# Optimization experiments

Measured on AMD Instinct MI355X. Metric: run time of the kernel, lower is better.

## Reference

```python
import jax, jax.numpy as jnp
from jax import lax
import numpy as np

B = 2048
NUM_COMPO = 650
NUM_CHARS = 27533
COMPO_SCORE_THRESH = 0.7
SCORE_ADJ_SCALE = 0.1
K = 10  # top-k chars and max padded hit indices


def setup_inputs() -> dict:
    key = jax.random.key(0)
    k1, k2, k3, k4, k5 = jax.random.split(key, 5)
    return {
        "pred_class_logits": jax.random.normal(k1, (B, NUM_CHARS), dtype=jnp.float32),
        "pred_compo_logits": jax.random.normal(k2, (B, NUM_COMPO), dtype=jnp.float32),
        "chinese_char_ids": jax.random.randint(k3, (B,), 0, NUM_CHARS, dtype=jnp.int32),
        "compo_co_occurrence_prob": jax.random.uniform(k4, (NUM_COMPO, NUM_COMPO), dtype=jnp.float32),
        "compo_chinese_matrix": jax.random.randint(k5, (NUM_COMPO, NUM_CHARS), 0, 2, dtype=jnp.int32),
    }


def _components_to_char(compo_scores, co_occ, matrix):
    """Per-sample: compo_scores [C], co_occ [C,C], matrix [C,V] (0/1 int)."""
    # score adjustment: sum over compos with score>0.88 of co_occ row * score * scale
    hi = compo_scores > 0.88
    w = jnp.where(hi, compo_scores, 0.0)                       # [C]
    adjusted = compo_scores + SCORE_ADJ_SCALE * (w @ co_occ)   # [C]
    max_idx = jnp.argmax(adjusted)
    max_score = compo_scores[max_idx]

    # select compos above threshold, sorted descending by score
    sel = compo_scores > COMPO_SCORE_THRESH
    num_sel = jnp.sum(sel.astype(jnp.int32))
    masked = jnp.where(sel, compo_scores, -jnp.inf)
    order = jnp.argsort(-masked)                                # selected first, desc
    sorted_scores = jnp.take(compo_scores, order)               # [C]

    hit0 = matrix[max_idx]                                      # [V] int

    def cond(st):
        i, hit, _prev = st
        return (i < num_sel) & (jnp.sum(hit) > 1)

    def body(st):
        i, hit, _prev = st
        comp = matrix[order[i]]
        new_hit = ((hit + comp) == 2).astype(hit.dtype)         # intersection
        return (i + 1, new_hit, hit)

    i, hit, prev = lax.while_loop(cond, body, (jnp.int32(1), hit0, hit0))
    num_hit = jnp.sum(hit)
    empty = num_hit == 0
    i = jnp.where(empty, i - 1, i)
    hit = jnp.where(empty, prev, hit)
    hit_score = jnp.where(i == 1, max_score, sorted_scores[i - 1])

    # first K indices where hit == 1, padded with -1 (fixed shape)
    ar = jnp.arange(NUM_CHARS, dtype=jnp.int32)
    vals = jnp.where(hit == 1, NUM_CHARS - ar, 0)
    topv, topi = lax.top_k(vals, K)
    hit_indices = jnp.where(topv > 0, topi.astype(jnp.int32), -1)
    return adjusted, hit_indices, hit_score


def reference(pred_class_logits, pred_compo_logits, chinese_char_ids,
              compo_co_occurrence_prob, compo_chinese_matrix):
    class_probs = jax.nn.softmax(pred_class_logits, axis=1)     # [B, V]
    compo_scores = jax.nn.sigmoid(pred_compo_logits)            # [B, C]
    class_scores, class_indices = lax.top_k(class_probs, K)     # [B, K]

    adjusted, hit_idx, hit_scores = jax.vmap(
        _components_to_char, in_axes=(0, None, None)
    )(compo_scores, compo_co_occurrence_prob, compo_chinese_matrix)

    num_hit = jnp.sum((hit_idx != -1).astype(jnp.int32), axis=1)  # [B]
    pred1 = jnp.where(num_hit == 1, hit_idx[:, 0], class_indices[:, 0])
    pred2 = jnp.where((class_scores[:, 0] < 0.85) & (num_hit == 1),
                      hit_idx[:, 0], class_indices[:, 0])

    hit_compare = jnp.any(class_indices[:, :, None] == hit_idx[:, None, :], axis=2)  # [B,K]
    j = jnp.argmax(hit_compare, axis=1)  # first True (all-False -> 0), matches stable desc argsort[0]
    pred3 = class_indices[jnp.arange(class_indices.shape[0]), j]

    return (class_indices, class_scores, compo_scores, adjusted,
            hit_idx, hit_scores, pred1, pred2, pred3)
```

## Files before the change

### kernel.cpp

```cpp
#include <hip/hip_runtime.h>
#include <math.h>

#define NB 2048
#define NC 650
#define NV 27533
#define NK 10
#define NWRD 861
#define NT 256
#define NCHUNK 11
#define CHPR 431
#define SVCAP 768

__global__ __launch_bounds__(NT) void pack_kernel(const int* __restrict__ mat,
                                                  unsigned* __restrict__ packed) {
  const int c = blockIdx.x >> 1;
  const int half = blockIdx.x & 1;
  const int lane = threadIdx.x & 63;
  const int w4 = threadIdx.x >> 6;
  const int ch0 = half ? 216 : 0;
  const int ch1 = half ? CHPR : 216;
  const int* row = mat + (size_t)c * NV;
  const size_t obase = (size_t)c * NWRD;

  int ch = ch0 + w4;
  int val = 0;
  if (ch < ch1) {
    int e = (ch << 6) + lane;
    val = (e < NV) ? row[e] : 0;
  }
  while (ch < ch1) {
    int chn = ch + 4;
    int valn = 0;
    if (chn < ch1) {
      int en = (chn << 6) + lane;
      valn = (en < NV) ? row[en] : 0;
    }
    unsigned long long m = __ballot(val != 0);
    if (lane < 2) {
      int wi = (ch << 1) + lane;
      if (wi < NWRD) packed[obase + wi] = (unsigned)(m >> (lane * 32));
    }
    val = valn;
    ch = chn;
  }
}

__device__ __forceinline__ int block_sum(int v, volatile int* red4, int tid) {
#pragma unroll
  for (int off = 32; off > 0; off >>= 1) v += __shfl_down(v, off);
  if ((tid & 63) == 0) red4[tid >> 6] = v;
  __syncthreads();
  int tot = red4[0] + red4[1] + red4[2] + red4[3];
  __syncthreads();
  return tot;
}

__global__ __launch_bounds__(NT, 8) void gen_pred_kernel(
    const float* __restrict__ class_logits,
    const float* __restrict__ compo_logits,
    const float* __restrict__ co_occ,
    const unsigned* __restrict__ packed,
    float* __restrict__ out) {
  const int b = blockIdx.x;
  const int tid = threadIdx.x;
  const int lane = tid & 63;
  const int wid = tid >> 6;

  __shared__ __align__(16) char arena[10464];
  float* s_sv_v = (float*)arena;
  int* s_sv_i = (int*)(arena + 3072);
  float* s_score = (float*)arena;
  int* s_selidx = (int*)(arena + 2608);
  int* s_hi = (int*)(arena + 5216);
  int* s_order = (int*)(arena + 7824);

  __shared__ float red_f[4];
  __shared__ float red_s[4];
  __shared__ int red_i[4];
  __shared__ int s_svcnt;
  __shared__ int s_cls_idx[NK];
  __shared__ float s_cls_sc[NK];
  __shared__ int s_hit[NK];
  __shared__ int s_hicnt[NCHUNK];
  __shared__ int s_selcnt[NCHUNK];

  const size_t o_cidx = 0;
  const size_t o_csc = (size_t)NB * NK;
  const size_t o_comp = 2 * (size_t)NB * NK;
  const size_t o_adj = o_comp + (size_t)NB * NC;
  const size_t o_hidx = o_adj + (size_t)NB * NC;
  const size_t o_hsc = o_hidx + (size_t)NB * NK;
  const size_t o_p1 = o_hsc + NB;
  const size_t o_p2 = o_p1 + NB;
  const size_t o_p3 = o_p2 + NB;

  const float* lg = class_logits + (size_t)b * NV;
  const int s0 = (4 - (b & 3)) & 3;
  const int M4 = (NV - s0) >> 2;
  const int baseT = s0 + (M4 << 2);
  const float4* lg4 = (const float4*)(lg + s0);

  float mx = -INFINITY;
  float ss0 = 0.f, ss1 = 0.f;
  if (tid < s0) { float x = lg[tid]; ss0 += __expf(x); mx = fmaxf(mx, x); }
  {
    int v = tid;
    float4 f;
    if (v < M4) f = lg4[v];
    while (v < M4) {
      int vn = v + NT;
      float4 fn = f;
      if (vn < M4) fn = lg4[vn];
      ss0 += __expf(f.x); ss1 += __expf(f.y);
      ss0 += __expf(f.z); ss1 += __expf(f.w);
      mx = fmaxf(mx, fmaxf(fmaxf(f.x, f.y), fmaxf(f.z, f.w)));
      f = fn; v = vn;
    }
  }
  if (tid < NV - baseT) { float x = lg[baseT + tid]; ss0 += __expf(x); mx = fmaxf(mx, x); }

  {
    float s = ss0 + ss1;
#pragma unroll
    for (int off = 32; off > 0; off >>= 1) s += __shfl_down(s, off);
    float g = mx;
    g = fmaxf(g, __shfl_xor(g, 1));
    g = fmaxf(g, __shfl_xor(g, 2));
    g = fmaxf(g, __shfl_xor(g, 4));
    g = fmaxf(g, __shfl_xor(g, 8));
    float t = fminf(g, __shfl_xor(g, 16));
    t = fminf(t, __shfl_xor(t, 32));
    if (lane == 0) { red_s[wid] = s; red_f[wid] = t; }
  }
  if (tid == 0) s_svcnt = 0;
  __syncthreads();
  const float Sv = red_s[0] + red_s[1] + red_s[2] + red_s[3];
  const float T = fminf(fminf(red_f[0], red_f[1]), fminf(red_f[2], red_f[3]));

#define SV_APPEND(pred, val, idxv)                                          \
  {                                                                         \
    bool p_ = (pred);                                                       \
    unsigned long long m_ = __ballot(p_);                                   \
    if (m_) {                                                               \
      int leader_ = (int)(__ffsll(m_) - 1);                                 \
      int base_ = 0;                                                        \
      if (lane == leader_) base_ = atomicAdd(&s_svcnt, (int)__popcll(m_));  \
      base_ = __shfl(base_, leader_);                                       \
      if (p_) {                                                             \
        int pos_ = base_ + (int)__popcll(m_ & ((1ull << lane) - 1ull));     \
        if (pos_ < SVCAP) { s_sv_v[pos_] = (val); s_sv_i[pos_] = (idxv); }  \
      }                                                                     \
    }                                                                       \
  }

  if (wid == 0) {
    bool p = (tid < s0) && (lg[tid] >= T);
    float v = (tid < s0) ? lg[tid] : 0.f;
    SV_APPEND(p, v, tid);
  }
  {
    int v = tid;
    float4 f;
    if (v < M4) f = lg4[v];
    while (v < M4) {
      int vn = v + NT;
      float4 fn = f;
      if (vn < M4) fn = lg4[vn];
      float m4 = fmaxf(fmaxf(f.x, f.y), fmaxf(f.z, f.w));
      if (__ballot(m4 >= T)) {
        int base = s0 + (v << 2);
        SV_APPEND(f.x >= T, f.x, base);
        SV_APPEND(f.y >= T, f.y, base + 1);
        SV_APPEND(f.z >= T, f.z, base + 2);
        SV_APPEND(f.w >= T, f.w, base + 3);
      }
      f = fn; v = vn;
    }
  }
  if (wid == 0) {
    int rem = NV - baseT;
    bool p = (tid < rem) && (lg[baseT + tid] >= T);
    float v = (tid < rem) ? lg[baseT + tid] : 0.f;
    SV_APPEND(p, v, baseT + tid);
  }
#undef SV_APPEND
  __syncthreads();

  {
    int S = s_svcnt;
    if (S > SVCAP) S = SVCAP;
    for (int t2 = tid; t2 < S; t2 += NT) {
      float vt = s_sv_v[t2];
      int it = s_sv_i[t2];
      int r = 0;
      for (int q = 0; q < S; q++) {
        float vq = s_sv_v[q];
        int iq = s_sv_i[q];
        r += (vq > vt || (vq == vt && iq < it)) ? 1 : 0;
      }
      if (r < NK) { s_cls_idx[r] = it; s_cls_sc[r] = vt; }
    }
  }
  __syncthreads();
  if (tid < NK) {
    int cidx = s_cls_idx[tid];
    float sc = __expf(s_cls_sc[tid]) / Sv;
    s_cls_sc[tid] = sc;
    out[o_cidx + (size_t)b * NK + tid] = (float)cidx;
    out[o_csc + (size_t)b * NK + tid] = sc;
  }

  const float* cl = compo_logits + (size_t)b * NC;
  for (int j = tid; j < NC; j += NT) {
    float x = cl[j];
    float sc = 1.f / (1.f + expf(-x));
    s_score[j] = sc;
    out[o_comp + (size_t)b * NC + j] = sc;
  }
  __syncthreads();

  for (int c = wid; c < NCHUNK; c += 4) {
    int e = (c << 6) + lane;
    float s = (e < NC) ? s_score[e] : 0.f;
    unsigned long long mh = __ballot(s > 0.88f);
    unsigned long long ms = __ballot(s > 0.7f);
    if (lane == 0) { s_hicnt[c] = __popcll(mh); s_selcnt[c] = __popcll(ms); }
  }
  __syncthreads();
  int nhi = 0, nsel = 0;
#pragma unroll
  for (int q = 0; q < NCHUNK; q++) { nhi += s_hicnt[q]; nsel += s_selcnt[q]; }
  for (int c = wid; c < NCHUNK; c += 4) {
    int e = (c << 6) + lane;
    float s = (e < NC) ? s_score[e] : 0.f;
    unsigned long long mh = __ballot(s > 0.88f);
    unsigned long long ms = __ballot(s > 0.7f);
    int oh = 0, os = 0;
    for (int q = 0; q < c; q++) { oh += s_hicnt[q]; os += s_selcnt[q]; }
    unsigned long long lower = (1ull << lane) - 1ull;
    if (s > 0.88f) s_hi[oh + __popcll(mh & lower)] = e;
    if (s > 0.7f) s_selidx[os + __popcll(ms & lower)] = e;
  }
  __syncthreads();

  for (int t = tid; t < nsel; t += NT) {
    int j = s_selidx[t];
    float sj = s_score[j];
    int r = 0;
    for (int q = 0; q < nsel; q++) {
      int jq = s_selidx[q];
      float sq = s_score[jq];
      r += (sq > sj || (sq == sj && jq < j)) ? 1 : 0;
    }
    s_order[r] = j;
  }

  float bestv = -INFINITY;
  int besti = 0x7fffffff;
  for (int j = tid; j < NC; j += NT) {
    float acc = 0.f;
    for (int h = 0; h < nhi; h++) {
      int i2 = s_hi[h];
      acc = fmaf(s_score[i2], co_occ[(size_t)i2 * NC + j], acc);
    }
    float adj = s_score[j] + 0.1f * acc;
    out[o_adj + (size_t)b * NC + j] = adj;
    if (adj > bestv || (adj == bestv && j < besti)) { bestv = adj; besti = j; }
  }
#pragma unroll
  for (int off = 32; off > 0; off >>= 1) {
    float ov = __shfl_down(bestv, off);
    int oi = __shfl_down(besti, off);
    if (ov > bestv || (ov == bestv && oi < besti)) { bestv = ov; besti = oi; }
  }
  if (lane == 0) { red_f[wid] = bestv; red_i[wid] = besti; }
  __syncthreads();
  int max_idx;
  {
    float bv = red_f[0]; int bi = red_i[0];
#pragma unroll
    for (int q = 1; q < 4; q++) {
      float qv = red_f[q]; int qi = red_i[q];
      if (qv > bv || (qv == bv && qi < bi)) { bv = qv; bi = qi; }
    }
    max_idx = bi;
  }
  const float max_score = s_score[max_idx];
  __syncthreads();

  unsigned hw[4], pv[4], pf[4];
  int cnt, cnt_prev, i;
  {
    const unsigned* prow = packed + (size_t)max_idx * NWRD;
    int pc = 0;
#pragma unroll
    for (int t = 0; t < 4; t++) {
      int w = (tid << 2) + t;
      unsigned x = (w < NWRD) ? prow[w] : 0u;
      hw[t] = x;
      pv[t] = x;
      pc += __popc(x);
    }
    if (1 < nsel) {
      const unsigned* row = packed + (size_t)s_order[1] * NWRD;
#pragma unroll
      for (int t = 0; t < 4; t++) {
        int w = (tid << 2) + t;
        pf[t] = (w < NWRD) ? row[w] : 0u;
      }
    }
    cnt = block_sum(pc, red_i, tid);
    cnt_prev = cnt;
    i = 1;
    while (i < nsel && cnt > 1) {
      unsigned nx[4];
      int p2 = 0;
#pragma unroll
      for (int t = 0; t < 4; t++) {
        unsigned x = hw[t] & pf[t];
        nx[t] = x;
        p2 += __popc(x);
      }
      int inext = i + 1;
      if (inext < nsel) {
        const unsigned* row = packed + (size_t)s_order[inext] * NWRD;
#pragma unroll
        for (int t = 0; t < 4; t++) {
          int w = (tid << 2) + t;
          pf[t] = (w < NWRD) ? row[w] : 0u;
        }
      }
      int nc2 = block_sum(p2, red_i, tid);
#pragma unroll
      for (int t = 0; t < 4; t++) { pv[t] = hw[t]; hw[t] = nx[t]; }
      cnt_prev = cnt;
      cnt = nc2;
      i = inext;
    }
    if (cnt == 0 && i > 1) {
      i--;
      cnt = cnt_prev;
#pragma unroll
      for (int t = 0; t < 4; t++) hw[t] = pv[t];
    }
  }

  if (tid < NK) s_hit[tid] = -1;
  {
    int myc = 0;
#pragma unroll
    for (int t = 0; t < 4; t++) myc += __popc(hw[t]);
    int inc = myc;
#pragma unroll
    for (int off = 1; off < 64; off <<= 1) {
      int y = __shfl_up(inc, off);
      if (lane >= off) inc += y;
    }
    if (lane == 63) red_i[wid] = inc;
    __syncthreads();
    int excl = inc - myc;
    for (int q = 0; q < wid; q++) excl += red_i[q];
    int r = excl;
    if (r < NK) {
#pragma unroll
      for (int t = 0; t < 4; t++) {
        unsigned x = hw[t];
        int wb = ((tid << 2) + t) << 5;
        while (x && r < NK) {
          int bpos = __ffs(x) - 1;
          x &= x - 1;
          s_hit[r] = wb + bpos;
          r++;
        }
        if (r >= NK) break;
      }
    }
  }
  __syncthreads();

  int num_hit = cnt < NK ? cnt : NK;
  if (tid < NK) out[o_hidx + (size_t)b * NK + tid] = (float)s_hit[tid];
  if (tid == 0) {
    float hsc = (i <= 1) ? max_score : s_score[s_order[i - 1]];
    out[o_hsc + b] = hsc;
    int ci0 = s_cls_idx[0];
    float cs0 = s_cls_sc[0];
    int h0 = s_hit[0];
    int p1 = (num_hit == 1) ? h0 : ci0;
    int p2 = (cs0 < 0.85f && num_hit == 1) ? h0 : ci0;
    int jj = 0;
    for (int k = 0; k < NK; k++) {
      bool m = false;
#pragma unroll
      for (int q = 0; q < NK; q++) m = m || (s_cls_idx[k] == s_hit[q]);
      if (m) { jj = k; break; }
    }
    out[o_p1 + b] = (float)p1;
    out[o_p2 + b] = (float)p2;
    out[o_p3 + b] = (float)s_cls_idx[jj];
  }
}

extern "C" void kernel_launch(void* const* d_in, const int* in_sizes, int n_in,
                              void* d_out, int out_size, void* d_ws, size_t ws_size,
                              hipStream_t stream) {
  const float* class_logits = (const float*)d_in[0];
  const float* compo_logits = (const float*)d_in[1];
  const float* co_occ = (const float*)d_in[3];
  const int* mat = (const int*)d_in[4];
  float* out = (float*)d_out;
  unsigned* packed = (unsigned*)d_ws;

  pack_kernel<<<2 * NC, NT, 0, stream>>>(mat, packed);
  gen_pred_kernel<<<NB, NT, 0, stream>>>(class_logits, compo_logits, co_occ,
                                         packed, out);
}
```

Baseline: 460.1 us.

## Fuse top-k candidate collection into softmax pass and rework packing and intersection

The pack kernel now reads the 0/1 matrix with int4 loads and builds bit words in shared memory with atomicOr. The softmax pass also collects top-k candidates above a fixed logit threshold, avoiding a second read of the logits, and falls back to an exact rescan when too few or too many candidates are found. The co-occurrence dot product gets four accumulators, and the hit-set intersection loop runs in a single wavefront with shuffle reductions instead of block-wide syncs. Occupancy hint drops from 8 to 6. The fixed threshold relies on the logit distribution, but the fallback keeps results correct.

```diff
diff --git a/kernel.cpp b/kernel.cpp
--- a/kernel.cpp
+++ b/kernel.cpp
@@ -8,54 +8,52 @@
 #define NWRD 861
 #define NT 256
 #define NCHUNK 11
-#define CHPR 431
 #define SVCAP 768
+#define T0 2.5f
 
 __global__ __launch_bounds__(NT) void pack_kernel(const int* __restrict__ mat,
                                                   unsigned* __restrict__ packed) {
-  const int c = blockIdx.x >> 1;
-  const int half = blockIdx.x & 1;
-  const int lane = threadIdx.x & 63;
-  const int w4 = threadIdx.x >> 6;
-  const int ch0 = half ? 216 : 0;
-  const int ch1 = half ? CHPR : 216;
-  const int* row = mat + (size_t)c * NV;
-  const size_t obase = (size_t)c * NWRD;
-
-  int ch = ch0 + w4;
-  int val = 0;
-  if (ch < ch1) {
-    int e = (ch << 6) + lane;
-    val = (e < NV) ? row[e] : 0;
-  }
-  while (ch < ch1) {
-    int chn = ch + 4;
-    int valn = 0;
-    if (chn < ch1) {
-      int en = (chn << 6) + lane;
-      valn = (en < NV) ? row[en] : 0;
-    }
-    unsigned long long m = __ballot(val != 0);
-    if (lane < 2) {
-      int wi = (ch << 1) + lane;
-      if (wi < NWRD) packed[obase + wi] = (unsigned)(m >> (lane * 32));
-    }
-    val = valn;
-    ch = chn;
-  }
+  const int c = blockIdx.x;
+  __shared__ unsigned s_w[NWRD];
+  for (int w = threadIdx.x; w < NWRD; w += NT) s_w[w] = 0;
+  __syncthreads();
+  const size_t rbeg = (size_t)c * NV;
+  const size_t g0 = rbeg & ~(size_t)3;
+  const int pre = (int)(rbeg - g0);
+  const int nchunks = (NV + pre + 3) >> 2;
+  const size_t NTOT = (size_t)NC * NV;
+  for (int t = threadIdx.x; t < nchunks; t += NT) {
+    size_t g = g0 + ((size_t)t << 2);
+    int4 q;
+    if (g + 4 <= NTOT) {
+      q = *(const int4*)(mat + g);
+    } else {
+      q.x = (g < NTOT) ? mat[g] : 0;
+      q.y = (g + 1 < NTOT) ? mat[g + 1] : 0;
+      q.z = (g + 2 < NTOT) ? mat[g + 2] : 0;
+      q.w = (g + 3 < NTOT) ? mat[g + 3] : 0;
+    }
+    long e0 = (long)g - (long)rbeg;
+    unsigned nib = 0;
+    if (q.x && e0 >= 0 && e0 < NV) nib |= 1u;
+    if (q.y && e0 + 1 >= 0 && e0 + 1 < NV) nib |= 2u;
+    if (q.z && e0 + 2 >= 0 && e0 + 2 < NV) nib |= 4u;
+    if (q.w && e0 + 3 >= 0 && e0 + 3 < NV) nib |= 8u;
+    if (nib) {
+      if (e0 < 0) { nib >>= (int)(-e0); e0 = 0; }
+      int w = (int)(e0 >> 5), sh = (int)(e0 & 31);
+      unsigned long long m = (unsigned long long)nib << sh;
+      atomicOr(&s_w[w], (unsigned)m);
+      unsigned hi = (unsigned)(m >> 32);
+      if (hi && w + 1 < NWRD) atomicOr(&s_w[w + 1], hi);
+    }
+  }
+  __syncthreads();
+  unsigned* orow = packed + (size_t)c * NWRD;
+  for (int w = threadIdx.x; w < NWRD; w += NT) orow[w] = s_w[w];
 }
 
-__device__ __forceinline__ int block_sum(int v, volatile int* red4, int tid) {
-#pragma unroll
-  for (int off = 32; off > 0; off >>= 1) v += __shfl_down(v, off);
-  if ((tid & 63) == 0) red4[tid >> 6] = v;
-  __syncthreads();
-  int tot = red4[0] + red4[1] + red4[2] + red4[3];
-  __syncthreads();
-  return tot;
-}
-
-__global__ __launch_bounds__(NT, 8) void gen_pred_kernel(
+__global__ __launch_bounds__(NT, 6) void gen_pred_kernel(
     const float* __restrict__ class_logits,
     const float* __restrict__ compo_logits,
     const float* __restrict__ co_occ,
@@ -73,11 +71,12 @@
   int* s_selidx = (int*)(arena + 2608);
   int* s_hi = (int*)(arena + 5216);
   int* s_order = (int*)(arena + 7824);
+  __shared__ unsigned s_words[NWRD];
 
   __shared__ float red_f[4];
   __shared__ float red_s[4];
   __shared__ int red_i[4];
-  __shared__ int s_svcnt;
+  __shared__ int s_svcnt, s_cnt, s_i;
   __shared__ int s_cls_idx[NK];
   __shared__ float s_cls_sc[NK];
   __shared__ int s_hit[NK];
@@ -100,24 +99,63 @@
   const int baseT = s0 + (M4 << 2);
   const float4* lg4 = (const float4*)(lg + s0);
 
-  float mx = -INFINITY;
-  float ss0 = 0.f, ss1 = 0.f;
-  if (tid < s0) { float x = lg[tid]; ss0 += __expf(x); mx = fmaxf(mx, x); }
+  if (tid == 0) s_svcnt = 0;
+  __syncthreads();
+
+  float mx = -INFINITY, ss0 = 0.f, ss1 = 0.f;
+
+#define APPEND1(x, e)                                                   \
+  { int p_ = atomicAdd(&s_svcnt, 1);                                    \
+    if (p_ < SVCAP) { s_sv_v[p_] = (x); s_sv_i[p_] = (e); } }
+
+  if (tid < s0) {
+    float x = lg[tid];
+    ss0 += __expf(x); mx = fmaxf(mx, x);
+    if (x >= T0) APPEND1(x, tid);
+  }
+  {
+    int rem = NV - baseT;
+    if (tid < rem) {
+      float x = lg[baseT + tid];
+      ss1 += __expf(x); mx = fmaxf(mx, x);
+      if (x >= T0) APPEND1(x, baseT + tid);
+    }
+  }
+
+#define PROC4(f, ebase)                                                  \
+  {                                                                      \
+    ss0 += __expf(f.x); ss1 += __expf(f.y);                              \
+    ss0 += __expf(f.z); ss1 += __expf(f.w);                              \
+    float m4_ = fmaxf(fmaxf(f.x, f.y), fmaxf(f.z, f.w));                 \
+    mx = fmaxf(mx, m4_);                                                 \
+    if (m4_ >= T0) {                                                     \
+      int e_ = (ebase);                                                  \
+      int c_ = (f.x >= T0) + (f.y >= T0) + (f.z >= T0) + (f.w >= T0);    \
+      int p_ = atomicAdd(&s_svcnt, c_);                                  \
+      if (f.x >= T0) { if (p_ < SVCAP) { s_sv_v[p_] = f.x; s_sv_i[p_] = e_; } p_++; }     \
+      if (f.y >= T0) { if (p_ < SVCAP) { s_sv_v[p_] = f.y; s_sv_i[p_] = e_ + 1; } p_++; } \
+      if (f.z >= T0) { if (p_ < SVCAP) { s_sv_v[p_] = f.z; s_sv_i[p_] = e_ + 2; } p_++; } \
+      if (f.w >= T0) { if (p_ < SVCAP) { s_sv_v[p_] = f.w; s_sv_i[p_] = e_ + 3; } p_++; } \
+    }                                                                    \
+  }
+
   {
     int v = tid;
-    float4 f;
-    if (v < M4) f = lg4[v];
+    float4 fa, fb;
+    bool hb = (v + NT) < M4;
+    if (v < M4) fa = lg4[v];
+    if (hb) fb = lg4[v + NT];
     while (v < M4) {
-      int vn = v + NT;
-      float4 fn = f;
-      if (vn < M4) fn = lg4[vn];
-      ss0 += __expf(f.x); ss1 += __expf(f.y);
-      ss0 += __expf(f.z); ss1 += __expf(f.w);
-      mx = fmaxf(mx, fmaxf(fmaxf(f.x, f.y), fmaxf(f.z, f.w)));
-      f = fn; v = vn;
-    }
-  }
-  if (tid < NV - baseT) { float x = lg[baseT + tid]; ss0 += __expf(x); mx = fmaxf(mx, x); }
+      int va = v + 2 * NT, vb = v + 3 * NT;
+      float4 fa2, fb2;
+      bool ha2 = va < M4, hb2 = vb < M4;
+      if (ha2) fa2 = lg4[va];
+      if (hb2) fb2 = lg4[vb];
+      PROC4(fa, s0 + (v << 2));
+      if (hb) PROC4(fb, s0 + ((v + NT) << 2));
+      fa = fa2; fb = fb2; hb = hb2; v = va;
+    }
+  }
 
   {
     float s = ss0 + ss1;
@@ -132,63 +170,37 @@
     t = fminf(t, __shfl_xor(t, 32));
     if (lane == 0) { red_s[wid] = s; red_f[wid] = t; }
   }
-  if (tid == 0) s_svcnt = 0;
   __syncthreads();
   const float Sv = red_s[0] + red_s[1] + red_s[2] + red_s[3];
   const float T = fminf(fminf(red_f[0], red_f[1]), fminf(red_f[2], red_f[3]));
-
-#define SV_APPEND(pred, val, idxv)                                          \
-  {                                                                         \
-    bool p_ = (pred);                                                       \
-    unsigned long long m_ = __ballot(p_);                                   \
-    if (m_) {                                                               \
-      int leader_ = (int)(__ffsll(m_) - 1);                                 \
-      int base_ = 0;                                                        \
-      if (lane == leader_) base_ = atomicAdd(&s_svcnt, (int)__popcll(m_));  \
-      base_ = __shfl(base_, leader_);                                       \
-      if (p_) {                                                             \
-        int pos_ = base_ + (int)__popcll(m_ & ((1ull << lane) - 1ull));     \
-        if (pos_ < SVCAP) { s_sv_v[pos_] = (val); s_sv_i[pos_] = (idxv); }  \
-      }                                                                     \
-    }                                                                       \
-  }
-
-  if (wid == 0) {
-    bool p = (tid < s0) && (lg[tid] >= T);
-    float v = (tid < s0) ? lg[tid] : 0.f;
-    SV_APPEND(p, v, tid);
-  }
-  {
-    int v = tid;
-    float4 f;
-    if (v < M4) f = lg4[v];
-    while (v < M4) {
-      int vn = v + NT;
-      float4 fn = f;
-      if (vn < M4) fn = lg4[vn];
-      float m4 = fmaxf(fmaxf(f.x, f.y), fmaxf(f.z, f.w));
-      if (__ballot(m4 >= T)) {
-        int base = s0 + (v << 2);
-        SV_APPEND(f.x >= T, f.x, base);
-        SV_APPEND(f.y >= T, f.y, base + 1);
-        SV_APPEND(f.z >= T, f.z, base + 2);
-        SV_APPEND(f.w >= T, f.w, base + 3);
-      }
-      f = fn; v = vn;
-    }
-  }
-  if (wid == 0) {
-    int rem = NV - baseT;
-    bool p = (tid < rem) && (lg[baseT + tid] >= T);
-    float v = (tid < rem) ? lg[baseT + tid] : 0.f;
-    SV_APPEND(p, v, baseT + tid);
-  }
-#undef SV_APPEND
-  __syncthreads();
-
-  {
-    int S = s_svcnt;
-    if (S > SVCAP) S = SVCAP;
+  int svc = s_svcnt;
+
+  if (svc < NK || svc > SVCAP) {
+    __syncthreads();
+    if (tid == 0) s_svcnt = 0;
+    __syncthreads();
+    if (tid < s0) { float x = lg[tid]; if (x >= T) APPEND1(x, tid); }
+    {
+      int rem = NV - baseT;
+      if (tid < rem) { float x = lg[baseT + tid]; if (x >= T) APPEND1(x, baseT + tid); }
+    }
+    for (int v = tid; v < M4; v += NT) {
+      float4 f = lg4[v];
+      int e = s0 + (v << 2);
+      if (f.x >= T) APPEND1(f.x, e);
+      if (f.y >= T) APPEND1(f.y, e + 1);
+      if (f.z >= T) APPEND1(f.z, e + 2);
+      if (f.w >= T) APPEND1(f.w, e + 3);
+    }
+    __syncthreads();
+    svc = s_svcnt;
+  }
+#undef APPEND1
+#undef PROC4
+  __syncthreads();
+
+  {
+    int S = svc < SVCAP ? svc : SVCAP;
     for (int t2 = tid; t2 < S; t2 += NT) {
       float vt = s_sv_v[t2];
       int it = s_sv_i[t2];
@@ -258,12 +270,24 @@
   float bestv = -INFINITY;
   int besti = 0x7fffffff;
   for (int j = tid; j < NC; j += NT) {
-    float acc = 0.f;
-    for (int h = 0; h < nhi; h++) {
-      int i2 = s_hi[h];
-      acc = fmaf(s_score[i2], co_occ[(size_t)i2 * NC + j], acc);
-    }
-    float adj = s_score[j] + 0.1f * acc;
+    float a0 = 0.f, a1 = 0.f, a2 = 0.f, a3 = 0.f;
+    int h = 0;
+    for (; h + 4 <= nhi; h += 4) {
+      int i0 = s_hi[h], i1 = s_hi[h + 1], i2 = s_hi[h + 2], i3 = s_hi[h + 3];
+      float c0 = co_occ[(size_t)i0 * NC + j];
+      float c1 = co_occ[(size_t)i1 * NC + j];
+      float c2 = co_occ[(size_t)i2 * NC + j];
+      float c3 = co_occ[(size_t)i3 * NC + j];
+      a0 = fmaf(s_score[i0], c0, a0);
+      a1 = fmaf(s_score[i1], c1, a1);
+      a2 = fmaf(s_score[i2], c2, a2);
+      a3 = fmaf(s_score[i3], c3, a3);
+    }
+    for (; h < nhi; h++) {
+      int ih = s_hi[h];
+      a0 = fmaf(s_score[ih], co_occ[(size_t)ih * NC + j], a0);
+    }
+    float adj = s_score[j] + 0.1f * ((a0 + a1) + (a2 + a3));
     out[o_adj + (size_t)b * NC + j] = adj;
     if (adj > bestv || (adj == bestv && j < besti)) { bestv = adj; besti = j; }
   }
@@ -288,68 +312,70 @@
   const float max_score = s_score[max_idx];
   __syncthreads();
 
-  unsigned hw[4], pv[4], pf[4];
-  int cnt, cnt_prev, i;
-  {
+  if (wid == 0) {
+    unsigned hw[14], pf[14];
     const unsigned* prow = packed + (size_t)max_idx * NWRD;
     int pc = 0;
 #pragma unroll
-    for (int t = 0; t < 4; t++) {
-      int w = (tid << 2) + t;
+    for (int t = 0; t < 14; t++) {
+      int w = (t << 6) + lane;
       unsigned x = (w < NWRD) ? prow[w] : 0u;
       hw[t] = x;
-      pv[t] = x;
       pc += __popc(x);
     }
-    if (1 < nsel) {
+#pragma unroll
+    for (int off = 32; off > 0; off >>= 1) pc += __shfl_down(pc, off);
+    int cnt = __shfl(pc, 0);
+    int i = 1;
+    if (nsel > 1) {
       const unsigned* row = packed + (size_t)s_order[1] * NWRD;
 #pragma unroll
-      for (int t = 0; t < 4; t++) {
-        int w = (tid << 2) + t;
+      for (int t = 0; t < 14; t++) {
+        int w = (t << 6) + lane;
         pf[t] = (w < NWRD) ? row[w] : 0u;
       }
     }
-    cnt = block_sum(pc, red_i, tid);
-    cnt_prev = cnt;
-    i = 1;
     while (i < nsel && cnt > 1) {
-      unsigned nx[4];
       int p2 = 0;
 #pragma unroll
-      for (int t = 0; t < 4; t++) {
-        unsigned x = hw[t] & pf[t];
-        nx[t] = x;
-        p2 += __popc(x);
-      }
-      int inext = i + 1;
-      if (inext < nsel) {
-        const unsigned* row = packed + (size_t)s_order[inext] * NWRD;
-#pragma unroll
-        for (int t = 0; t < 4; t++) {
-          int w = (tid << 2) + t;
+      for (int t = 0; t < 14; t++) p2 += __popc(hw[t] & pf[t]);
+#pragma unroll
+      for (int off = 32; off > 0; off >>= 1) p2 += __shfl_down(p2, off);
+      int np = __shfl(p2, 0);
+      if (np == 0) break;
+#pragma unroll
+      for (int t = 0; t < 14; t++) hw[t] &= pf[t];
+      cnt = np;
+      i++;
+      if (i < nsel) {
+        const unsigned* row = packed + (size_t)s_order[i] * NWRD;
+#pragma unroll
+        for (int t = 0; t < 14; t++) {
+          int w = (t << 6) + lane;
           pf[t] = (w < NWRD) ? row[w] : 0u;
         }
       }
-      int nc2 = block_sum(p2, red_i, tid);
-#pragma unroll
-      for (int t = 0; t < 4; t++) { pv[t] = hw[t]; hw[t] = nx[t]; }
-      cnt_prev = cnt;
-      cnt = nc2;
-      i = inext;
-    }
-    if (cnt == 0 && i > 1) {
-      i--;
-      cnt = cnt_prev;
-#pragma unroll
-      for (int t = 0; t < 4; t++) hw[t] = pv[t];
-    }
-  }
+    }
+#pragma unroll
+    for (int t = 0; t < 14; t++) {
+      int w = (t << 6) + lane;
+      if (w < NWRD) s_words[w] = hw[t];
+    }
+    if (lane == 0) { s_cnt = cnt; s_i = i; }
+  }
+  __syncthreads();
 
   if (tid < NK) s_hit[tid] = -1;
   {
+    unsigned wv[4];
     int myc = 0;
 #pragma unroll
-    for (int t = 0; t < 4; t++) myc += __popc(hw[t]);
+    for (int t = 0; t < 4; t++) {
+      int w = (tid << 2) + t;
+      unsigned x = (w < NWRD) ? s_words[w] : 0u;
+      wv[t] = x;
+      myc += __popc(x);
+    }
     int inc = myc;
 #pragma unroll
     for (int off = 1; off < 64; off <<= 1) {
@@ -364,7 +390,7 @@
     if (r < NK) {
 #pragma unroll
       for (int t = 0; t < 4; t++) {
-        unsigned x = hw[t];
+        unsigned x = wv[t];
         int wb = ((tid << 2) + t) << 5;
         while (x && r < NK) {
           int bpos = __ffs(x) - 1;
@@ -378,26 +404,29 @@
   }
   __syncthreads();
 
-  int num_hit = cnt < NK ? cnt : NK;
-  if (tid < NK) out[o_hidx + (size_t)b * NK + tid] = (float)s_hit[tid];
-  if (tid == 0) {
-    float hsc = (i <= 1) ? max_score : s_score[s_order[i - 1]];
-    out[o_hsc + b] = hsc;
-    int ci0 = s_cls_idx[0];
-    float cs0 = s_cls_sc[0];
-    int h0 = s_hit[0];
-    int p1 = (num_hit == 1) ? h0 : ci0;
-    int p2 = (cs0 < 0.85f && num_hit == 1) ? h0 : ci0;
-    int jj = 0;
-    for (int k = 0; k < NK; k++) {
-      bool m = false;
-#pragma unroll
-      for (int q = 0; q < NK; q++) m = m || (s_cls_idx[k] == s_hit[q]);
-      if (m) { jj = k; break; }
-    }
-    out[o_p1 + b] = (float)p1;
-    out[o_p2 + b] = (float)p2;
-    out[o_p3 + b] = (float)s_cls_idx[jj];
+  {
+    int cnt = s_cnt, i = s_i;
+    int num_hit = cnt < NK ? cnt : NK;
+    if (tid < NK) out[o_hidx + (size_t)b * NK + tid] = (float)s_hit[tid];
+    if (tid == 0) {
+      float hsc = (i <= 1) ? max_score : s_score[s_order[i - 1]];
+      out[o_hsc + b] = hsc;
+      int ci0 = s_cls_idx[0];
+      float cs0 = s_cls_sc[0];
+      int h0 = s_hit[0];
+      int p1 = (num_hit == 1) ? h0 : ci0;
+      int p2 = (cs0 < 0.85f && num_hit == 1) ? h0 : ci0;
+      int jj = 0;
+      for (int k = 0; k < NK; k++) {
+        bool m = false;
+#pragma unroll
+        for (int q = 0; q < NK; q++) m = m || (s_cls_idx[k] == s_hit[q]);
+        if (m) { jj = k; break; }
+      }
+      out[o_p1 + b] = (float)p1;
+      out[o_p2 + b] = (float)p2;
+      out[o_p3 + b] = (float)s_cls_idx[jj];
+    }
   }
 }
 
@@ -411,7 +440,7 @@
   float* out = (float*)d_out;
   unsigned* packed = (unsigned*)d_ws;
 
-  pack_kernel<<<2 * NC, NT, 0, stream>>>(mat, packed);
+  pack_kernel<<<NC, NT, 0, stream>>>(mat, packed);
   gen_pred_kernel<<<NB, NT, 0, stream>>>(class_logits, compo_logits, co_occ,
                                          packed, out);
 }
```

After: 450.8 us. 1.02x faster.
